# Performance work log

Measured on AMD Instinct MI355X. Metric: run time of the kernel, lower is better.

Reference implementation:

```python
import jax, jax.numpy as jnp
import numpy as np

ALPHA = 5.0
EPS = 1e-12  # avoids inf grad of sqrt at the self-distance (exact 0)


def setup_inputs() -> dict:
    key = jax.random.key(0)
    xyz = jax.random.normal(key, (4, 8192, 3), dtype=jnp.float32)
    return {"xyz": xyz, "nbr_size": 2}


def reference(xyz, nbr_size):
    # Brute-force KNN of xyz against itself (self is included with dist 0,
    # matching pointops.knn(query, ref) when query == ref).
    sq = jnp.sum(xyz * xyz, axis=-1)                      # (B, N)
    # squared pairwise distances: ||a||^2 + ||b||^2 - 2 a.b  -> (B, N, N)
    d2 = sq[:, :, None] + sq[:, None, :] - 2.0 * jnp.einsum(
        'bnd,bmd->bnm', xyz, xyz)
    neg_top, _idx = jax.lax.top_k(-d2, nbr_size)          # (B, N, k) smallest d2
    dist = jnp.sqrt(jnp.maximum(-neg_top, EPS))           # Euclidean distance
    dsum = dist.sum(-1)                                   # (B, N)
    avg_dist = dsum.mean(-1, keepdims=True)               # (B, 1)
    # loss = sum of per-point distance sums exceeding alpha * mean
    loss = jnp.where(dsum > avg_dist * ALPHA, dsum, 0.0).sum()
    return loss
```

## Files before the change

### kernel.cpp

```cpp
#include <hip/hip_runtime.h>

#define BB 4
#define NN 8192
#define BN (BB * NN)
#define ALPHA 5.0f
#define EPSF 1e-12f
#define BLOCK 256
#define QPT 4
#define QB (BLOCK * QPT)
#define BIGF 1e30f

__global__ __launch_bounds__(BLOCK) void prep_kernel(
    const float* __restrict__ xyz, float4* __restrict__ refs4) {
  int g = blockIdx.x * BLOCK + threadIdx.x;
  float x = xyz[3 * g + 0], y = xyz[3 * g + 1], z = xyz[3 * g + 2];
  float hpp = 0.5f * fmaf(x, x, fmaf(y, y, z * z));
  refs4[g] = make_float4(x, y, z, hpp);
}

template <int NSEG>
__global__ __launch_bounds__(BLOCK, 8) void knn_kernel(
    const float4* __restrict__ refs4, float2* __restrict__ pairs) {
  constexpr int SEG = NN / NSEG;
  constexpr int CHUNKS = NN / QB;
  constexpr int U = 8;
  int bid = blockIdx.x;
  int s = bid % NSEG;
  int rem = bid / NSEG;
  int qchunk = rem % CHUNKS;
  int b = rem / CHUNKS;

  const float4* __restrict__ qb4 = refs4 + (size_t)b * NN;

  float nqx[QPT], nqy[QPT], nqz[QPT], hq[QPT], m1[QPT], m2[QPT];
#pragma unroll
  for (int i = 0; i < QPT; i++) {
    int q = qchunk * QB + threadIdx.x + i * BLOCK;
    float4 qp = qb4[q];
    nqx[i] = -qp.x;
    nqy[i] = -qp.y;
    nqz[i] = -qp.z;
    hq[i] = qp.w;
    m1[i] = BIGF;
    m2[i] = BIGF;
  }

  const float4* __restrict__ rp = qb4 + s * SEG;
  float4 cur[U];
#pragma unroll
  for (int u = 0; u < U; u++) cur[u] = rp[u];

  for (int j0 = 0; j0 < SEG; j0 += U) {
    int jn = (j0 + U < SEG) ? (j0 + U) : 0;
    float4 nxt[U];
#pragma unroll
    for (int u = 0; u < U; u++) nxt[u] = rp[jn + u];

#pragma unroll
    for (int u = 0; u < U; u++) {
      float4 p = cur[u];
      float pw = p.w;
#pragma unroll
      for (int i = 0; i < QPT; i++) {
        float t = fmaf(nqx[i], p.x, pw);
        t = fmaf(nqy[i], p.y, t);
        t = fmaf(nqz[i], p.z, t);
        m2[i] = __builtin_amdgcn_fmed3f(t, m1[i], m2[i]);
        m1[i] = fminf(m1[i], t);
      }
    }
#pragma unroll
    for (int u = 0; u < U; u++) cur[u] = nxt[u];
  }

#pragma unroll
  for (int i = 0; i < QPT; i++) {
    int q = qchunk * QB + threadIdx.x + i * BLOCK;
    pairs[(size_t)s * BN + b * NN + q] =
        make_float2(m1[i] + hq[i], m2[i] + hq[i]);
  }
}

#define MBLK 128
#define NPART (BN / MBLK)
template <int NSEG>
__global__ __launch_bounds__(MBLK) void merge_kernel(
    const float2* __restrict__ pairs, float* __restrict__ dsum,
    float* __restrict__ partial) {
  int g = blockIdx.x * MBLK + threadIdx.x;
  float m1 = BIGF, m2 = BIGF;
#pragma unroll 8
  for (int s = 0; s < NSEG; s++) {
    float2 p = pairs[(size_t)s * BN + g];
    float n2 = __builtin_amdgcn_fmed3f(p.x, m1, m2);
    m1 = fminf(m1, p.x);
    m2 = n2;
    n2 = __builtin_amdgcn_fmed3f(p.y, m1, m2);
    m1 = fminf(m1, p.y);
    m2 = n2;
  }
  float ds = sqrtf(fmaxf(m1 + m1, EPSF)) + sqrtf(fmaxf(m2 + m2, EPSF));
  dsum[g] = ds;

  float v = ds;
#pragma unroll
  for (int off = 32; off > 0; off >>= 1) v += __shfl_down(v, off, 64);
  __shared__ float warp_sums[MBLK / 64];
  if ((threadIdx.x & 63) == 0) warp_sums[threadIdx.x >> 6] = v;
  __syncthreads();
  if (threadIdx.x == 0) {
    float t = 0.0f;
#pragma unroll
    for (int w = 0; w < MBLK / 64; w++) t += warp_sums[w];
    partial[blockIdx.x] = t;
  }
}

#define LBLK 1024
__global__ __launch_bounds__(LBLK) void loss_kernel(
    const float* __restrict__ dsum, const float* __restrict__ partial,
    float* __restrict__ out) {
  __shared__ float s_avg[BB];
  if (threadIdx.x < NPART) {
    float v = partial[threadIdx.x];
#pragma unroll
    for (int off = 32; off > 0; off >>= 1) v += __shfl_down(v, off, 64);
    if ((threadIdx.x & 63) == 0) s_avg[threadIdx.x >> 6] = v * (ALPHA / NN);
  }
  __syncthreads();

  const float4* d4 = (const float4*)dsum;
  float acc = 0.0f;
#pragma unroll
  for (int it = 0; it < BN / (LBLK * 4); it++) {
    int idx = it * LBLK + threadIdx.x;
    float4 v = d4[idx];
    float thr = s_avg[idx >> 11];
    acc += (v.x > thr) ? v.x : 0.0f;
    acc += (v.y > thr) ? v.y : 0.0f;
    acc += (v.z > thr) ? v.z : 0.0f;
    acc += (v.w > thr) ? v.w : 0.0f;
  }
#pragma unroll
  for (int off = 32; off > 0; off >>= 1) acc += __shfl_down(acc, off, 64);
  __shared__ float warp_sums[LBLK / 64];
  if ((threadIdx.x & 63) == 0) warp_sums[threadIdx.x >> 6] = acc;
  __syncthreads();
  if (threadIdx.x == 0) {
    float t = 0.0f;
#pragma unroll
    for (int w = 0; w < LBLK / 64; w++) t += warp_sums[w];
    out[0] = t;
  }
}

template <int NSEG>
static void run(const float* xyz, float* out, void* d_ws, hipStream_t stream) {
  float2* pairs = (float2*)d_ws;
  float4* refs4 = (float4*)(pairs + (size_t)NSEG * BN);
  float* dsum = (float*)(refs4 + BN);
  float* partial = dsum + BN;
  prep_kernel<<<BN / BLOCK, BLOCK, 0, stream>>>(xyz, refs4);
  int grid1 = BB * (NN / QB) * NSEG;
  knn_kernel<NSEG><<<grid1, BLOCK, 0, stream>>>(refs4, pairs);
  merge_kernel<NSEG><<<BN / MBLK, MBLK, 0, stream>>>(pairs, dsum, partial);
  loss_kernel<<<1, LBLK, 0, stream>>>(dsum, partial, out);
}

extern "C" void kernel_launch(void* const* d_in, const int* in_sizes, int n_in,
                              void* d_out, int out_size, void* d_ws,
                              size_t ws_size, hipStream_t stream) {
  const float* xyz = (const float*)d_in[0];
  float* out = (float*)d_out;

  auto need = [](int nseg) {
    return (size_t)nseg * BN * sizeof(float2) + BN * sizeof(float4) +
           BN * sizeof(float) + NPART * sizeof(float);
  };
  if (ws_size >= need(64)) {
    run<64>(xyz, out, d_ws, stream);
  } else if (ws_size >= need(32)) {
    run<32>(xyz, out, d_ws, stream);
  } else {
    run<16>(xyz, out, d_ws, stream);
  }
}
```

Before: 98.62 us.

## Exploit guaranteed self-neighbor to track only nearest non-self distance

Since the query set equals the reference set and k is 2, the smallest distance is always the self-distance. The KNN kernel therefore tracks only the running minimum with v_min3 over pairs of candidates. Top-2 tracking is kept only in the block whose segment contains the query itself, and the self entry is dropped there. The merge pass then reads one float per segment instead of a pair and adds the constant sqrt(EPS) term for self. This cuts ALU work per pair and halves the intermediate traffic. The risk is small numerical differences from assuming the self-distance clamps exactly to EPS.

```diff
diff --git a/kernel.cpp b/kernel.cpp
--- a/kernel.cpp
+++ b/kernel.cpp
@@ -10,6 +10,12 @@
 #define QB (BLOCK * QPT)
 #define BIGF 1e30f
 
+__device__ __forceinline__ float fmin3f(float a, float b, float c) {
+  float d;
+  asm("v_min3_f32 %0, %1, %2, %3" : "=v"(d) : "v"(a), "v"(b), "v"(c));
+  return d;
+}
+
 __global__ __launch_bounds__(BLOCK) void prep_kernel(
     const float* __restrict__ xyz, float4* __restrict__ refs4) {
   int g = blockIdx.x * BLOCK + threadIdx.x;
@@ -20,7 +26,7 @@
 
 template <int NSEG>
 __global__ __launch_bounds__(BLOCK, 8) void knn_kernel(
-    const float4* __restrict__ refs4, float2* __restrict__ pairs) {
+    const float4* __restrict__ refs4, float* __restrict__ pairs) {
   constexpr int SEG = NN / NSEG;
   constexpr int CHUNKS = NN / QB;
   constexpr int U = 8;
@@ -46,38 +52,72 @@
   }
 
   const float4* __restrict__ rp = qb4 + s * SEG;
+  const bool self_block = ((s * SEG) / QB) == qchunk;
+
   float4 cur[U];
 #pragma unroll
   for (int u = 0; u < U; u++) cur[u] = rp[u];
 
-  for (int j0 = 0; j0 < SEG; j0 += U) {
-    int jn = (j0 + U < SEG) ? (j0 + U) : 0;
-    float4 nxt[U];
-#pragma unroll
-    for (int u = 0; u < U; u++) nxt[u] = rp[jn + u];
-
-#pragma unroll
-    for (int u = 0; u < U; u++) {
-      float4 p = cur[u];
-      float pw = p.w;
-#pragma unroll
-      for (int i = 0; i < QPT; i++) {
-        float t = fmaf(nqx[i], p.x, pw);
-        t = fmaf(nqy[i], p.y, t);
-        t = fmaf(nqz[i], p.z, t);
-        m2[i] = __builtin_amdgcn_fmed3f(t, m1[i], m2[i]);
-        m1[i] = fminf(m1[i], t);
+  if (!self_block) {
+    for (int j0 = 0; j0 < SEG; j0 += U) {
+      int jn = (j0 + U < SEG) ? (j0 + U) : 0;
+      float4 nxt[U];
+#pragma unroll
+      for (int u = 0; u < U; u++) nxt[u] = rp[jn + u];
+
+#pragma unroll
+      for (int u = 0; u < U; u += 2) {
+        float4 p0 = cur[u], p1 = cur[u + 1];
+        float pw0 = p0.w, pw1 = p1.w;
+#pragma unroll
+        for (int i = 0; i < QPT; i++) {
+          float t0 = fmaf(nqx[i], p0.x, pw0);
+          t0 = fmaf(nqy[i], p0.y, t0);
+          t0 = fmaf(nqz[i], p0.z, t0);
+          float t1 = fmaf(nqx[i], p1.x, pw1);
+          t1 = fmaf(nqy[i], p1.y, t1);
+          t1 = fmaf(nqz[i], p1.z, t1);
+          m1[i] = fmin3f(m1[i], t0, t1);
+        }
       }
+#pragma unroll
+      for (int u = 0; u < U; u++) cur[u] = nxt[u];
     }
-#pragma unroll
-    for (int u = 0; u < U; u++) cur[u] = nxt[u];
+  } else {
+    for (int j0 = 0; j0 < SEG; j0 += U) {
+      int jn = (j0 + U < SEG) ? (j0 + U) : 0;
+      float4 nxt[U];
+#pragma unroll
+      for (int u = 0; u < U; u++) nxt[u] = rp[jn + u];
+
+#pragma unroll
+      for (int u = 0; u < U; u += 2) {
+        float4 p0 = cur[u], p1 = cur[u + 1];
+        float pw0 = p0.w, pw1 = p1.w;
+#pragma unroll
+        for (int i = 0; i < QPT; i++) {
+          float t0 = fmaf(nqx[i], p0.x, pw0);
+          t0 = fmaf(nqy[i], p0.y, t0);
+          t0 = fmaf(nqz[i], p0.z, t0);
+          float t1 = fmaf(nqx[i], p1.x, pw1);
+          t1 = fmaf(nqy[i], p1.y, t1);
+          t1 = fmaf(nqz[i], p1.z, t1);
+          float med = __builtin_amdgcn_fmed3f(m1[i], t0, t1);
+          m2[i] = fminf(m2[i], med);
+          m1[i] = fmin3f(m1[i], t0, t1);
+        }
+      }
+#pragma unroll
+      for (int u = 0; u < U; u++) cur[u] = nxt[u];
+    }
   }
 
 #pragma unroll
   for (int i = 0; i < QPT; i++) {
     int q = qchunk * QB + threadIdx.x + i * BLOCK;
-    pairs[(size_t)s * BN + b * NN + q] =
-        make_float2(m1[i] + hq[i], m2[i] + hq[i]);
+    float best = m1[i];
+    if (self_block && (q / SEG) == s) best = m2[i];
+    pairs[(size_t)s * BN + b * NN + q] = best + hq[i];
   }
 }
 
@@ -85,21 +125,17 @@
 #define NPART (BN / MBLK)
 template <int NSEG>
 __global__ __launch_bounds__(MBLK) void merge_kernel(
-    const float2* __restrict__ pairs, float* __restrict__ dsum,
+    const float* __restrict__ pairs, float* __restrict__ dsum,
     float* __restrict__ partial) {
   int g = blockIdx.x * MBLK + threadIdx.x;
-  float m1 = BIGF, m2 = BIGF;
+  float m = BIGF;
 #pragma unroll 8
-  for (int s = 0; s < NSEG; s++) {
-    float2 p = pairs[(size_t)s * BN + g];
-    float n2 = __builtin_amdgcn_fmed3f(p.x, m1, m2);
-    m1 = fminf(m1, p.x);
-    m2 = n2;
-    n2 = __builtin_amdgcn_fmed3f(p.y, m1, m2);
-    m1 = fminf(m1, p.y);
-    m2 = n2;
-  }
-  float ds = sqrtf(fmaxf(m1 + m1, EPSF)) + sqrtf(fmaxf(m2 + m2, EPSF));
+  for (int s = 0; s < NSEG; s += 2) {
+    float a = pairs[(size_t)s * BN + g];
+    float c = pairs[(size_t)(s + 1) * BN + g];
+    m = fmin3f(m, a, c);
+  }
+  float ds = sqrtf(fmaxf(m + m, EPSF)) + sqrtf(EPSF);
   dsum[g] = ds;
 
   float v = ds;
@@ -156,7 +192,7 @@
 
 template <int NSEG>
 static void run(const float* xyz, float* out, void* d_ws, hipStream_t stream) {
-  float2* pairs = (float2*)d_ws;
+  float* pairs = (float*)d_ws;
   float4* refs4 = (float4*)(pairs + (size_t)NSEG * BN);
   float* dsum = (float*)(refs4 + BN);
   float* partial = dsum + BN;
@@ -174,7 +210,7 @@
   float* out = (float*)d_out;
 
   auto need = [](int nseg) {
-    return (size_t)nseg * BN * sizeof(float2) + BN * sizeof(float4) +
+    return (size_t)nseg * BN * sizeof(float) + BN * sizeof(float4) +
            BN * sizeof(float) + NPART * sizeof(float);
   };
   if (ws_size >= need(64)) {
```

Measured after the change: 97.43 us (median of 2 runs). Within noise of the previous version (-1.2%).
